# Optimization experiments

Measured on AMD Instinct MI355X. Metric: run time of the kernel, lower is better.

The kernel has to match this reference:

```python
import jax, jax.numpy as jnp
import numpy as np

VOCAB = 50000
D = 512          # in_feat == word_embedding_dim
B = 4096
S = 128
NUM_LABELS = 3


def setup_inputs() -> dict:
    key = jax.random.key(0)
    ks = jax.random.split(key, 16)
    ids_a = jax.random.randint(ks[0], (B, S), 0, VOCAB, dtype=jnp.int32)
    ids_b = jax.random.randint(ks[1], (B, S), 0, VOCAB, dtype=jnp.int32)
    mask_a = jax.random.randint(ks[2], (B, S), 0, 2) > 0
    mask_b = jax.random.randint(ks[3], (B, S), 0, 2) > 0
    s = 0.02
    W_emb = jax.random.normal(ks[4], (VOCAB, D), jnp.float32) * s
    W_emb = W_emb.at[0].set(0.0)  # padding_idx=0
    enc_w1 = jax.random.normal(ks[5], (D, D), jnp.float32) * s
    enc_b1 = jnp.zeros((D,), jnp.float32)
    enc_w2 = jax.random.normal(ks[6], (D, D), jnp.float32) * s
    enc_b2 = jnp.zeros((D,), jnp.float32)
    cls_w1 = jax.random.normal(ks[7], (2 * D, D), jnp.float32) * s
    cls_b1 = jnp.zeros((D,), jnp.float32)
    cls_w2 = jax.random.normal(ks[8], (D, NUM_LABELS), jnp.float32) * s
    cls_b2 = jnp.zeros((NUM_LABELS,), jnp.float32)
    return {
        "text_a_inputs_id": ids_a, "text_b_inputs_id": ids_b,
        "text_a_attention_mask": mask_a, "text_b_attention_mask": mask_b,
        "W_emb": W_emb,
        "enc_w1": enc_w1, "enc_b1": enc_b1, "enc_w2": enc_w2, "enc_b2": enc_b2,
        "cls_w1": cls_w1, "cls_b1": cls_b1, "cls_w2": cls_w2, "cls_b2": cls_b2,
    }


def _encode(ids, mask, W_emb, w1, b1, w2, b2):
    # embedding gather [B,S,D], fused masked sum-pool -> [B,D]
    emb = W_emb[ids]
    pooled = jnp.einsum("bsd,bs->bd", emb, mask.astype(emb.dtype))
    x = jnp.tanh(pooled @ w1 + b1)
    x = jnp.tanh(x @ w2 + b2)  # dropout is identity in eval
    return x


def reference(text_a_inputs_id, text_b_inputs_id, text_a_attention_mask,
              text_b_attention_mask, W_emb, enc_w1, enc_b1, enc_w2, enc_b2,
              cls_w1, cls_b1, cls_w2, cls_b2):
    va = _encode(text_a_inputs_id, text_a_attention_mask, W_emb, enc_w1, enc_b1, enc_w2, enc_b2)
    vb = _encode(text_b_inputs_id, text_b_attention_mask, W_emb, enc_w1, enc_b1, enc_w2, enc_b2)
    pooled = jnp.concatenate([va, vb], axis=-1)  # [B, 2D]
    h = jnp.tanh(pooled @ cls_w1 + cls_b1)
    logits = h @ cls_w2 + cls_b2  # [B, num_labels]
    return logits
```

## Files before the change

kernel.cpp:

```cpp
#include <hip/hip_runtime.h>


typedef unsigned short u16;
typedef __attribute__((ext_vector_type(8))) short short8;
typedef __attribute__((ext_vector_type(4))) float f32x4;

__device__ __forceinline__ float bfu2f(u16 u) {
    union { unsigned int i; float f; } v;
    v.i = ((unsigned int)u) << 16;
    return v.f;
}

__device__ __forceinline__ u16 f2bfu(float f) {
    union { float f; unsigned int i; } v;
    v.f = f;
    unsigned int x = v.i;
    x += 0x7fffu + ((x >> 16) & 1u);
    return (u16)(x >> 16);
}

__device__ __forceinline__ float fast_tanh(float x) {
    float xc = fminf(fmaxf(x, -15.f), 15.f);
    float e = __builtin_amdgcn_exp2f(xc * 2.885390082f);
    return (e - 1.f) / (e + 1.f);
}

__device__ __forceinline__ int detect_wave(const u16* __restrict__ W,
                                           const unsigned int* __restrict__ m,
                                           int lane)
{
    int cnt = 0;
    int w01 = 1, b01 = 1, lo16 = 0;
    #pragma unroll
    for (int j = lane; j < 256; j += 64) {
        u16 u = W[1024 + 2 * j];
        int e = (u >> 7) & 0xFF;
        cnt += (e >= 0x6A && e <= 0x7E) ? 1 : 0;
        unsigned int v = m[j];
        w01 &= (v <= 1u) ? 1 : 0;
        b01 &= ((v & ~0x01010101u) == 0u) ? 1 : 0;
        lo16 |= ((v & 0xFFFFu) == 0x3F80u) ? 1 : 0;
    }
    #pragma unroll
    for (int off = 32; off > 0; off >>= 1) {
        cnt  += __shfl_down(cnt, off);
        w01  &= __shfl_down(w01, off);
        b01  &= __shfl_down(b01, off);
        lo16 |= __shfl_down(lo16, off);
    }
    int mtype;
    if (w01)        mtype = 0;
    else if (b01)   mtype = 1;
    else if (lo16)  mtype = 2;
    else            mtype = 3;
    int fl = ((cnt >= 128) ? 1 : 0) | (mtype << 2);
    return __shfl(fl, 0);
}

__device__ __forceinline__ int mask_nonzero(const void* __restrict__ msk,
                                            int idx, int mtype)
{
    switch (mtype) {
        case 0:  return ((const int*)msk)[idx] != 0;
        case 1:  return ((const unsigned char*)msk)[idx] != 0;
        case 2:  return ((const u16*)msk)[idx] != 0;
        default: return ((const unsigned int*)msk)[idx] != 0u;
    }
}

__global__ __launch_bounds__(128) void pool_kernel(
    const int* __restrict__ ids_a, const int* __restrict__ ids_b,
    const void* __restrict__ mska, const void* __restrict__ mskb,
    const void* __restrict__ W, u16* __restrict__ P,
    const unsigned int* __restrict__ Mdet)
{
    __shared__ int s_ids[128];
    __shared__ int s_cnt;
    __shared__ int s_flags;
    __shared__ float sP[512];
    const int t = threadIdx.x;
    const int w = t >> 6;
    const int lane = t & 63;

    if (t == 0) s_cnt = 0;
    if (t < 64) {
        int fl = detect_wave((const u16*)W, Mdet, t);
        if (t == 0) s_flags = fl;
    }
    __syncthreads();
    const int  flags = s_flags;
    const bool isbf  = (flags & 1) != 0;
    const int  mtype = (flags >> 2) & 3;

    const int row = blockIdx.x;
    const int r   = row & 4095;
    const int* __restrict__ ids = (row < 4096) ? ids_a : ids_b;
    const void* __restrict__ msk = (row < 4096) ? mska : mskb;

    int id = ids[r * 128 + t];
    int mk = mask_nonzero(msk, r * 128 + t, mtype);
    if (mk) {
        int idx = atomicAdd(&s_cnt, 1);
        s_ids[idx] = id;
    }
    __syncthreads();
    const int cnt = s_cnt;

    float acc[8] = {};
    if (isbf) {
        const u16* Wb = (const u16*)W;
        int j = w;
        for (; j + 6 < cnt; j += 8) {
            union { uint4 v; u16 s[8]; } r0, r1, r2, r3;
            r0.v = *(const uint4*)(Wb + (size_t)s_ids[j + 0] * 512 + lane * 8);
            r1.v = *(const uint4*)(Wb + (size_t)s_ids[j + 2] * 512 + lane * 8);
            r2.v = *(const uint4*)(Wb + (size_t)s_ids[j + 4] * 512 + lane * 8);
            r3.v = *(const uint4*)(Wb + (size_t)s_ids[j + 6] * 512 + lane * 8);
            #pragma unroll
            for (int i = 0; i < 8; ++i)
                acc[i] += bfu2f(r0.s[i]) + bfu2f(r1.s[i]) +
                          bfu2f(r2.s[i]) + bfu2f(r3.s[i]);
        }
        for (; j < cnt; j += 2) {
            union { uint4 v; u16 s[8]; } rr;
            rr.v = *(const uint4*)(Wb + (size_t)s_ids[j] * 512 + lane * 8);
            #pragma unroll
            for (int i = 0; i < 8; ++i) acc[i] += bfu2f(rr.s[i]);
        }
    } else {
        const float* Wf = (const float*)W;
        for (int j = w; j < cnt; j += 2) {
            const float* rp = Wf + (size_t)s_ids[j] * 512 + lane * 8;
            float4 a = *(const float4*)(rp + 0);
            float4 b = *(const float4*)(rp + 4);
            acc[0] += a.x; acc[1] += a.y; acc[2] += a.z; acc[3] += a.w;
            acc[4] += b.x; acc[5] += b.y; acc[6] += b.z; acc[7] += b.w;
        }
    }

    if (w == 0) {
        #pragma unroll
        for (int i = 0; i < 8; ++i) sP[lane * 8 + i] = acc[i];
    }
    __syncthreads();
    if (w == 1) {
        union { uint4 v; u16 s[8]; } o;
        #pragma unroll
        for (int i = 0; i < 8; ++i)
            o.s[i] = f2bfu(acc[i] + sP[lane * 8 + i]);
        *(uint4*)(P + (size_t)row * 512 + lane * 8) = o.v;
    }
}

template<bool ISBF>
__device__ __forceinline__ void gemm_body(
    const u16* __restrict__ A, const u16* __restrict__ A2, int K1,
    const void* __restrict__ Bv, const void* __restrict__ biasv,
    u16* __restrict__ C, int N, int K,
    u16* __restrict__ As0, u16* __restrict__ Bs0)
{
    const int tid  = threadIdx.x;
    const int lane = tid & 63;
    const int wid = tid >> 6;
    const int wm  = (wid & 3) * 32;
    const int wn  = (wid >> 2) * 32;
    const int ar = tid >> 2;
    const int ak = (tid & 3) * 8;
    const int bk = tid >> 3;
    const int jn = tid & 7;
    const int nb = jn * 8;
    const int bofs = (((bk >> 3) + jn) & 3) * 8 + (bk & 7);
    const int lm = lane & 15;
    const int kq = lane >> 4;
    const int kc = kq * 8;
    const int m0 = blockIdx.x * 128;
    const int n0 = blockIdx.y * 64;

    const u16*   Bb = (const u16*)Bv;
    const float* Bf = (const float*)Bv;

    f32x4 acc[2][2];
    #pragma unroll
    for (int i = 0; i < 2; ++i)
        #pragma unroll
        for (int j = 0; j < 2; ++j)
            acc[i][j] = (f32x4){0.f, 0.f, 0.f, 0.f};

    uint4 ra;
    uint4 rbb;
    float4 rf0, rf1;

    #define FETCH(k0)                                                         \
    {                                                                         \
        const int kg = (k0) + ak;                                             \
        const u16* base = (kg < K1) ? (A + kg) : (A2 + (kg - K1));            \
        ra = *(const uint4*)(base + (size_t)(m0 + ar) * 512);                 \
        if (tid < 256) {                                                      \
            if constexpr (ISBF) {                                             \
                rbb = *(const uint4*)(Bb + (size_t)((k0) + bk) * N + n0 + nb);\
            } else {                                                          \
                const float* Bp = Bf + (size_t)((k0) + bk) * N + n0 + nb;     \
                rf0 = *(const float4*)(Bp + 0);                               \
                rf1 = *(const float4*)(Bp + 4);                               \
            }                                                                 \
        }                                                                     \
    }

    #define STORE(pp)                                                         \
    {                                                                         \
        *(uint4*)&As0[(pp) * 5120 + ar * 40 + ak] = ra;                       \
        if (tid < 256) {                                                      \
            u16 bvals[8];                                                     \
            if constexpr (ISBF) {                                             \
                union { uint4 v; u16 s[8]; } ub; ub.v = rbb;                  \
                _Pragma("unroll")                                             \
                for (int i = 0; i < 8; ++i) bvals[i] = ub.s[i];               \
            } else {                                                          \
                bvals[0] = f2bfu(rf0.x); bvals[1] = f2bfu(rf0.y);             \
                bvals[2] = f2bfu(rf0.z); bvals[3] = f2bfu(rf0.w);             \
                bvals[4] = f2bfu(rf1.x); bvals[5] = f2bfu(rf1.y);             \
                bvals[6] = f2bfu(rf1.z); bvals[7] = f2bfu(rf1.w);             \
            }                                                                 \
            _Pragma("unroll")                                                 \
            for (int i = 0; i < 8; ++i)                                       \
                Bs0[(pp) * 2560 + (nb + i) * 40 + bofs] = bvals[i];           \
        }                                                                     \
    }

    FETCH(0)
    STORE(0)
    FETCH(32)
    __syncthreads();

    int p = 0;
    for (int k0 = 0; k0 < K; k0 += 32) {
        if (k0 + 32 < K) {
            STORE(p ^ 1)
            if (k0 + 64 < K) FETCH(k0 + 64)
        }

        const u16* Ap = As0 + p * 5120;
        const u16* Bp2 = Bs0 + p * 2560;
        short8 af[2], bf[2];
        #pragma unroll
        for (int i = 0; i < 2; ++i)
            af[i] = *(const short8*)&Ap[(wm + i * 16 + lm) * 40 + kc];
        #pragma unroll
        for (int j = 0; j < 2; ++j) {
            const int n = wn + j * 16 + lm;
            const int ch = ((kq + (n >> 3)) & 3) * 8;
            bf[j] = *(const short8*)&Bp2[n * 40 + ch];
        }
        #pragma unroll
        for (int i = 0; i < 2; ++i)
            #pragma unroll
            for (int j = 0; j < 2; ++j)
                acc[i][j] = __builtin_amdgcn_mfma_f32_16x16x32_bf16(
                    af[i], bf[j], acc[i][j], 0, 0, 0);

        if (k0 + 32 < K) __syncthreads();
        p ^= 1;
    }
    #undef FETCH
    #undef STORE

    #pragma unroll
    for (int j = 0; j < 2; ++j) {
        const int n = n0 + wn + j * 16 + lm;
        const float bsv = ISBF ? bfu2f(((const u16*)biasv)[n])
                               : ((const float*)biasv)[n];
        #pragma unroll
        for (int i = 0; i < 2; ++i) {
            #pragma unroll
            for (int r = 0; r < 4; ++r) {
                const int m = m0 + wm + i * 16 + kq * 4 + r;
                C[(size_t)m * N + n] = f2bfu(fast_tanh(acc[i][j][r] + bsv));
            }
        }
    }
}

__global__ __launch_bounds__(512, 4) void gemm_mfma(
    const u16* __restrict__ A, const u16* __restrict__ A2, int K1,
    const void* __restrict__ B, const void* __restrict__ bias,
    u16* __restrict__ C, int N, int K,
    const u16* __restrict__ Wdet, const unsigned int* __restrict__ Mdet)
{
    __shared__ __align__(16) u16 As[2 * 128 * 40];
    __shared__ __align__(16) u16 Bs[2 * 64 * 40];
    __shared__ int s_flags;

    if (threadIdx.x < 64) {
        int fl = detect_wave(Wdet, Mdet, threadIdx.x);
        if (threadIdx.x == 0) s_flags = fl;
    }
    __syncthreads();
    if (s_flags & 1) gemm_body<true >(A, A2, K1, B, bias, C, N, K, As, Bs);
    else             gemm_body<false>(A, A2, K1, B, bias, C, N, K, As, Bs);
}

__global__ __launch_bounds__(64) void logits_kernel(
    const u16* __restrict__ H, const void* __restrict__ W2,
    const void* __restrict__ b2, float* __restrict__ out,
    const u16* __restrict__ Wdet, const unsigned int* __restrict__ Mdet)
{
    const int lane = threadIdx.x;
    const int fl = detect_wave(Wdet, Mdet, lane);
    const bool isbf = (fl & 1) != 0;

    const int m = blockIdx.x;
    union { uint4 v; u16 s[8]; } h;
    h.v = *(const uint4*)(H + (size_t)m * 512 + lane * 8);

    float a0 = 0.f, a1 = 0.f, a2 = 0.f;
    #pragma unroll
    for (int i = 0; i < 8; ++i) {
        const int k = lane * 8 + i;
        float x = bfu2f(h.s[i]);
        float w0, w1, w2;
        if (isbf) {
            const u16* Wb = (const u16*)W2;
            w0 = bfu2f(Wb[k * 3 + 0]); w1 = bfu2f(Wb[k * 3 + 1]); w2 = bfu2f(Wb[k * 3 + 2]);
        } else {
            const float* Wf = (const float*)W2;
            w0 = Wf[k * 3 + 0]; w1 = Wf[k * 3 + 1]; w2 = Wf[k * 3 + 2];
        }
        a0 += x * w0; a1 += x * w1; a2 += x * w2;
    }
    #pragma unroll
    for (int off = 32; off > 0; off >>= 1) {
        a0 += __shfl_down(a0, off);
        a1 += __shfl_down(a1, off);
        a2 += __shfl_down(a2, off);
    }
    if (lane == 0) {
        float b0, b1, b2v;
        if (isbf) {
            const u16* bb = (const u16*)b2;
            b0 = bfu2f(bb[0]); b1 = bfu2f(bb[1]); b2v = bfu2f(bb[2]);
        } else {
            const float* bf = (const float*)b2;
            b0 = bf[0]; b1 = bf[1]; b2v = bf[2];
        }
        out[m * 3 + 0] = a0 + b0;
        out[m * 3 + 1] = a1 + b1;
        out[m * 3 + 2] = a2 + b2v;
    }
}

extern "C" void kernel_launch(void* const* d_in, const int* in_sizes, int n_in,
                              void* d_out, int out_size, void* d_ws, size_t ws_size,
                              hipStream_t stream)
{
    const int* ids_a  = (const int*)d_in[0];
    const int* ids_b  = (const int*)d_in[1];
    const void* mask_a = d_in[2];
    const void* mask_b = d_in[3];
    const void* W_emb  = d_in[4];
    const void* enc_w1 = d_in[5];
    const void* enc_b1 = d_in[6];
    const void* enc_w2 = d_in[7];
    const void* enc_b2 = d_in[8];
    const void* cls_w1 = d_in[9];
    const void* cls_b1 = d_in[10];
    const void* cls_w2 = d_in[11];
    const void* cls_b2 = d_in[12];

    const u16* Wdet = (const u16*)W_emb;
    const unsigned int* Mdet = (const unsigned int*)mask_a;

    u16* buf0 = (u16*)d_ws;
    u16* buf1 = buf0 + (size_t)8192 * 512;

    pool_kernel<<<8192, 128, 0, stream>>>(ids_a, ids_b, mask_a, mask_b,
                                          W_emb, buf0, Mdet);

    gemm_mfma<<<dim3(64, 8), 512, 0, stream>>>(
        buf0, buf0, 512, enc_w1, enc_b1, buf1, 512, 512, Wdet, Mdet);

    gemm_mfma<<<dim3(64, 8), 512, 0, stream>>>(
        buf1, buf1, 512, enc_w2, enc_b2, buf0, 512, 512, Wdet, Mdet);

    gemm_mfma<<<dim3(32, 8), 512, 0, stream>>>(
        buf0, buf0 + (size_t)4096 * 512, 512, cls_w1, cls_b1, buf1, 512, 1024, Wdet, Mdet);

    logits_kernel<<<4096, 64, 0, stream>>>(buf1, cls_w2, cls_b2, (float*)d_out, Wdet, Mdet);
}
```

Before: 357.4 us.

## Fuse encoder and classifier GEMMs and logits into one cooperative kernel

Replaces the three GEMM launches and the logits launch with a single cooperative kernel that runs each stage over a 512-block grid separated by grid-wide syncs. It targets per-launch overhead and the idle gaps between dependent small kernels. It adds grid.sync costs, requires all blocks to be co-resident, and leaves half the blocks idle during the classifier GEMM. The old multi-launch path is kept as a fallback if the cooperative launch fails.

```diff
diff --git a/kernel.cpp b/kernel.cpp
--- a/kernel.cpp
+++ b/kernel.cpp
@@ -1,4 +1,7 @@
 #include <hip/hip_runtime.h>
+#include <hip/hip_cooperative_groups.h>
+
+namespace cg = cooperative_groups;
 
 
 typedef unsigned short u16;
@@ -153,10 +156,10 @@
 }
 
 template<bool ISBF>
-__device__ __forceinline__ void gemm_body(
-    const u16* __restrict__ A, const u16* __restrict__ A2, int K1,
+__device__ __forceinline__ void gemm_tile(
+    const u16* __restrict__ A, const u16* __restrict__ A2, const int K1,
     const void* __restrict__ Bv, const void* __restrict__ biasv,
-    u16* __restrict__ C, int N, int K,
+    u16* __restrict__ C, const int K, const int m0, const int n0,
     u16* __restrict__ As0, u16* __restrict__ Bs0)
 {
     const int tid  = threadIdx.x;
@@ -173,8 +176,6 @@
     const int lm = lane & 15;
     const int kq = lane >> 4;
     const int kc = kq * 8;
-    const int m0 = blockIdx.x * 128;
-    const int n0 = blockIdx.y * 64;
 
     const u16*   Bb = (const u16*)Bv;
     const float* Bf = (const float*)Bv;
@@ -197,9 +198,9 @@
         ra = *(const uint4*)(base + (size_t)(m0 + ar) * 512);                 \
         if (tid < 256) {                                                      \
             if constexpr (ISBF) {                                             \
-                rbb = *(const uint4*)(Bb + (size_t)((k0) + bk) * N + n0 + nb);\
+                rbb = *(const uint4*)(Bb + (size_t)((k0) + bk) * 512 + n0 + nb);\
             } else {                                                          \
-                const float* Bp = Bf + (size_t)((k0) + bk) * N + n0 + nb;     \
+                const float* Bp = Bf + (size_t)((k0) + bk) * 512 + n0 + nb;   \
                 rf0 = *(const float4*)(Bp + 0);                               \
                 rf1 = *(const float4*)(Bp + 4);                               \
             }                                                                 \
@@ -274,16 +275,114 @@
             #pragma unroll
             for (int r = 0; r < 4; ++r) {
                 const int m = m0 + wm + i * 16 + kq * 4 + r;
-                C[(size_t)m * N + n] = f2bfu(fast_tanh(acc[i][j][r] + bsv));
+                C[(size_t)m * 512 + n] = f2bfu(fast_tanh(acc[i][j][r] + bsv));
             }
         }
     }
+}
+
+template<bool ISBF>
+__device__ __forceinline__ void fused_body(
+    const void* __restrict__ w1, const void* __restrict__ b1,
+    const void* __restrict__ w2, const void* __restrict__ b2,
+    const void* __restrict__ cw1, const void* __restrict__ cb1,
+    const void* __restrict__ cw2, const void* __restrict__ cb2,
+    u16* __restrict__ buf0, u16* __restrict__ buf1,
+    float* __restrict__ out, u16* As, u16* Bs)
+{
+    cg::grid_group grid = cg::this_grid();
+    const int bid = blockIdx.x;
+    const int tid = threadIdx.x;
+    const int m0 = (bid & 63) * 128;
+    const int n0 = (bid >> 6) * 64;
+
+    const u16* src = buf0;
+    u16*       dst = buf1;
+    #pragma unroll 1
+    for (int s = 0; s < 2; ++s) {
+        const void* ww = s ? w2 : w1;
+        const void* bb = s ? b2 : b1;
+        gemm_tile<ISBF>(src, src, 512, ww, bb, dst, 512, m0, n0, As, Bs);
+        __threadfence();
+        grid.sync();
+        const u16* t = src; src = dst; dst = (u16*)t;
+    }
+
+    if (bid < 256)
+        gemm_tile<ISBF>(buf0, buf0 + (size_t)4096 * 512, 512, cw1, cb1,
+                        buf1, 1024, (bid & 31) * 128, (bid >> 5) * 64, As, Bs);
+    __threadfence();
+    grid.sync();
+
+    const int lane = tid & 63;
+    const int m = bid * 8 + (tid >> 6);
+    union { uint4 v; u16 s[8]; } h;
+    h.v = *(const uint4*)(buf1 + (size_t)m * 512 + lane * 8);
+
+    float a0 = 0.f, a1 = 0.f, a2 = 0.f;
+    #pragma unroll
+    for (int i = 0; i < 8; ++i) {
+        const int k = lane * 8 + i;
+        float x = bfu2f(h.s[i]);
+        float v0, v1, v2;
+        if constexpr (ISBF) {
+            const u16* Wb = (const u16*)cw2;
+            v0 = bfu2f(Wb[k * 3 + 0]); v1 = bfu2f(Wb[k * 3 + 1]); v2 = bfu2f(Wb[k * 3 + 2]);
+        } else {
+            const float* Wf = (const float*)cw2;
+            v0 = Wf[k * 3 + 0]; v1 = Wf[k * 3 + 1]; v2 = Wf[k * 3 + 2];
+        }
+        a0 += x * v0; a1 += x * v1; a2 += x * v2;
+    }
+    #pragma unroll
+    for (int off = 32; off > 0; off >>= 1) {
+        a0 += __shfl_down(a0, off);
+        a1 += __shfl_down(a1, off);
+        a2 += __shfl_down(a2, off);
+    }
+    if (lane == 0) {
+        float c0, c1, c2;
+        if constexpr (ISBF) {
+            const u16* bb = (const u16*)cb2;
+            c0 = bfu2f(bb[0]); c1 = bfu2f(bb[1]); c2 = bfu2f(bb[2]);
+        } else {
+            const float* bf = (const float*)cb2;
+            c0 = bf[0]; c1 = bf[1]; c2 = bf[2];
+        }
+        out[m * 3 + 0] = a0 + c0;
+        out[m * 3 + 1] = a1 + c1;
+        out[m * 3 + 2] = a2 + c2;
+    }
+}
+
+__global__ __launch_bounds__(512, 4) void fused_enc(
+    const void* __restrict__ w1, const void* __restrict__ b1,
+    const void* __restrict__ w2, const void* __restrict__ b2,
+    const void* __restrict__ cw1, const void* __restrict__ cb1,
+    const void* __restrict__ cw2, const void* __restrict__ cb2,
+    u16* __restrict__ buf0, u16* __restrict__ buf1,
+    float* __restrict__ out,
+    const u16* __restrict__ Wdet, const unsigned int* __restrict__ Mdet)
+{
+    __shared__ __align__(16) u16 As[2 * 128 * 40];
+    __shared__ __align__(16) u16 Bs[2 * 64 * 40];
+    __shared__ int s_flags;
+
+    if (threadIdx.x < 64) {
+        int fl = detect_wave(Wdet, Mdet, threadIdx.x);
+        if (threadIdx.x == 0) s_flags = fl;
+    }
+    __syncthreads();
+    if (s_flags & 1)
+        fused_body<true >(w1, b1, w2, b2, cw1, cb1, cw2, cb2, buf0, buf1, out, As, Bs);
+    else
+        fused_body<false>(w1, b1, w2, b2, cw1, cb1, cw2, cb2, buf0, buf1, out, As, Bs);
 }
 
 __global__ __launch_bounds__(512, 4) void gemm_mfma(
     const u16* __restrict__ A, const u16* __restrict__ A2, int K1,
     const void* __restrict__ B, const void* __restrict__ bias,
-    u16* __restrict__ C, int N, int K,
+    u16* __restrict__ C, int K,
     const u16* __restrict__ Wdet, const unsigned int* __restrict__ Mdet)
 {
     __shared__ __align__(16) u16 As[2 * 128 * 40];
@@ -295,8 +394,10 @@
         if (threadIdx.x == 0) s_flags = fl;
     }
     __syncthreads();
-    if (s_flags & 1) gemm_body<true >(A, A2, K1, B, bias, C, N, K, As, Bs);
-    else             gemm_body<false>(A, A2, K1, B, bias, C, N, K, As, Bs);
+    const int m0 = blockIdx.x * 128;
+    const int n0 = blockIdx.y * 64;
+    if (s_flags & 1) gemm_tile<true >(A, A2, K1, B, bias, C, K, m0, n0, As, Bs);
+    else             gemm_tile<false>(A, A2, K1, B, bias, C, K, m0, n0, As, Bs);
 }
 
 __global__ __launch_bounds__(64) void logits_kernel(
@@ -371,18 +472,28 @@
 
     u16* buf0 = (u16*)d_ws;
     u16* buf1 = buf0 + (size_t)8192 * 512;
+    float* outp = (float*)d_out;
 
     pool_kernel<<<8192, 128, 0, stream>>>(ids_a, ids_b, mask_a, mask_b,
                                           W_emb, buf0, Mdet);
 
-    gemm_mfma<<<dim3(64, 8), 512, 0, stream>>>(
-        buf0, buf0, 512, enc_w1, enc_b1, buf1, 512, 512, Wdet, Mdet);
-
-    gemm_mfma<<<dim3(64, 8), 512, 0, stream>>>(
-        buf1, buf1, 512, enc_w2, enc_b2, buf0, 512, 512, Wdet, Mdet);
-
-    gemm_mfma<<<dim3(32, 8), 512, 0, stream>>>(
-        buf0, buf0 + (size_t)4096 * 512, 512, cls_w1, cls_b1, buf1, 512, 1024, Wdet, Mdet);
-
-    logits_kernel<<<4096, 64, 0, stream>>>(buf1, cls_w2, cls_b2, (float*)d_out, Wdet, Mdet);
-}
+    void* args[13] = {
+        (void*)&enc_w1, (void*)&enc_b1, (void*)&enc_w2, (void*)&enc_b2,
+        (void*)&cls_w1, (void*)&cls_b1, (void*)&cls_w2, (void*)&cls_b2,
+        (void*)&buf0,   (void*)&buf1,   (void*)&outp,
+        (void*)&Wdet,   (void*)&Mdet
+    };
+    hipError_t err = hipLaunchCooperativeKernel(
+        (const void*)fused_enc, dim3(512, 1, 1), dim3(512, 1, 1),
+        args, 0, stream);
+
+    if (err != hipSuccess) {
+        gemm_mfma<<<dim3(64, 8), 512, 0, stream>>>(
+            buf0, buf0, 512, enc_w1, enc_b1, buf1, 512, Wdet, Mdet);
+        gemm_mfma<<<dim3(64, 8), 512, 0, stream>>>(
+            buf1, buf1, 512, enc_w2, enc_b2, buf0, 512, Wdet, Mdet);
+        gemm_mfma<<<dim3(32, 8), 512, 0, stream>>>(
+            buf0, buf0 + (size_t)4096 * 512, 512, cls_w1, cls_b1, buf1, 1024, Wdet, Mdet);
+        logits_kernel<<<4096, 64, 0, stream>>>(buf1, cls_w2, cls_b2, outp, Wdet, Mdet);
+    }
+}
```

After: 840.6 us. 2.35x slower.

## Fuse both encoder GEMMs per row block and fold logits into classifier GEMM

Applied to the files above, without the earlier changes.

Replaces the two separate encoder GEMM launches with one kernel. Each 32-row block holds its pooled rows in registers, computes the first layer into LDS-staged fragments, then the second layer, and writes the result back in place. The classifier GEMM now computes tanh and the 3-wide logit projection in its epilogue and accumulates into a pre-zeroed output with atomics, which removes the hidden-state round trip and the separate logits kernel. In exchange, each block re-reads the full weight matrices and the encoder grid is smaller (256 blocks of 32 rows), so it has less parallelism and more weight traffic. The atomic accumulation also makes the float summation order nondeterministic.

```diff
diff --git a/kernel.cpp b/kernel.cpp
--- a/kernel.cpp
+++ b/kernel.cpp
@@ -153,10 +153,165 @@
 }
 
 template<bool ISBF>
-__device__ __forceinline__ void gemm_body(
-    const u16* __restrict__ A, const u16* __restrict__ A2, int K1,
+__device__ __forceinline__ void enc12_body(
+    u16* __restrict__ P,
+    const void* __restrict__ w1v, const void* __restrict__ b1v,
+    const void* __restrict__ w2v, const void* __restrict__ b2v,
+    u16* __restrict__ Bs, u16* __restrict__ Xbuf)
+{
+    const int tid  = threadIdx.x;
+    const int lane = tid & 63;
+    const int wid  = tid >> 6;
+    const int wm   = (wid & 1) * 16;
+    const int wn   = (wid >> 1) * 16;
+    const int lm   = lane & 15;
+    const int kq   = lane >> 4;
+    const int kc   = kq * 8;
+    const int R0   = blockIdx.x * 32;
+
+    const int bk = tid >> 3;
+    const int jn = tid & 7;
+    const int nb = jn * 8;
+
+    const u16*   b1b = (const u16*)b1v; const float* b1f = (const float*)b1v;
+    const u16*   b2b = (const u16*)b2v; const float* b2f = (const float*)b2v;
+
+    short8 af[16];
+    {
+        const u16* arow = P + (size_t)(R0 + wm + lm) * 512 + kc;
+        #pragma unroll
+        for (int s = 0; s < 16; ++s)
+            af[s] = *(const short8*)(arow + s * 32);
+    }
+    short8 af2[16];
+
+    const u16* Wb; const float* Wf;
+    uint4 rb0, rb1;
+    float4 rf00, rf01, rf10, rf11;
+
+#define FETCHW(k0, n0)                                                        \
+    {                                                                         \
+        const int kr0 = (k0) + bk;                                            \
+        const int kr1 = (k0) + bk + 64;                                       \
+        if constexpr (ISBF) {                                                 \
+            rb0 = *(const uint4*)(Wb + (size_t)kr0 * 512 + (n0) + nb);        \
+            rb1 = *(const uint4*)(Wb + (size_t)kr1 * 512 + (n0) + nb);        \
+        } else {                                                              \
+            const float* p0_ = Wf + (size_t)kr0 * 512 + (n0) + nb;            \
+            const float* p1_ = Wf + (size_t)kr1 * 512 + (n0) + nb;            \
+            rf00 = *(const float4*)p0_; rf01 = *(const float4*)(p0_ + 4);     \
+            rf10 = *(const float4*)p1_; rf11 = *(const float4*)(p1_ + 4);     \
+        }                                                                     \
+    }
+
+#define STOREW(pp)                                                            \
+    {                                                                         \
+        u16 bv0[8], bv1[8];                                                   \
+        if constexpr (ISBF) {                                                 \
+            union { uint4 v; u16 s[8]; } u0_, u1_;                            \
+            u0_.v = rb0; u1_.v = rb1;                                         \
+            _Pragma("unroll")                                                 \
+            for (int i = 0; i < 8; ++i) { bv0[i] = u0_.s[i]; bv1[i] = u1_.s[i]; } \
+        } else {                                                              \
+            bv0[0]=f2bfu(rf00.x); bv0[1]=f2bfu(rf00.y);                       \
+            bv0[2]=f2bfu(rf00.z); bv0[3]=f2bfu(rf00.w);                       \
+            bv0[4]=f2bfu(rf01.x); bv0[5]=f2bfu(rf01.y);                       \
+            bv0[6]=f2bfu(rf01.z); bv0[7]=f2bfu(rf01.w);                       \
+            bv1[0]=f2bfu(rf10.x); bv1[1]=f2bfu(rf10.y);                       \
+            bv1[2]=f2bfu(rf10.z); bv1[3]=f2bfu(rf10.w);                       \
+            bv1[4]=f2bfu(rf11.x); bv1[5]=f2bfu(rf11.y);                       \
+            bv1[6]=f2bfu(rf11.z); bv1[7]=f2bfu(rf11.w);                       \
+        }                                                                     \
+        const int o0_ = ((((bk >> 3) + jn) & 15)) * 8 + (bk & 7);             \
+        const int o1_ = ((((bk >> 3) + 8 + jn) & 15)) * 8 + (bk & 7);         \
+        _Pragma("unroll")                                                     \
+        for (int i = 0; i < 8; ++i) {                                         \
+            Bs[(pp) * 8704 + (nb + i) * 136 + o0_] = bv0[i];                  \
+            Bs[(pp) * 8704 + (nb + i) * 136 + o1_] = bv1[i];                  \
+        }                                                                     \
+    }
+
+#define KLOOP(afin)                                                           \
+    FETCHW(0, n0) STOREW(0) FETCHW(128, n0)                                   \
+    __syncthreads();                                                          \
+    _Pragma("unroll")                                                         \
+    for (int kb = 0; kb < 4; ++kb) {                                          \
+        const int p_ = kb & 1;                                                \
+        if (kb < 3) { STOREW(p_ ^ 1) if (kb < 2) FETCHW((kb + 2) * 128, n0) } \
+        _Pragma("unroll")                                                     \
+        for (int s = 0; s < 4; ++s) {                                         \
+            const int n_ = wn + lm;                                           \
+            const int ch = (((s * 4 + kq) + (n_ >> 3)) & 15) * 8;             \
+            short8 bf = *(const short8*)&Bs[p_ * 8704 + n_ * 136 + ch];       \
+            acc = __builtin_amdgcn_mfma_f32_16x16x32_bf16(afin[kb * 4 + s],   \
+                                                          bf, acc, 0, 0, 0);  \
+        }                                                                     \
+        if (kb < 3) __syncthreads();                                          \
+    }
+
+    Wb = (const u16*)w1v; Wf = (const float*)w1v;
+    #pragma unroll
+    for (int t = 0; t < 8; ++t) {
+        const int n0 = t * 64;
+        f32x4 acc = (f32x4){0.f, 0.f, 0.f, 0.f};
+        KLOOP(af)
+        const int   ncol = n0 + wn + lm;
+        const float bia  = ISBF ? bfu2f(b1b[ncol]) : b1f[ncol];
+        u16* xw = Xbuf + (t & 1) * (32 * 72);
+        #pragma unroll
+        for (int r = 0; r < 4; ++r)
+            xw[(wm + kq * 4 + r) * 72 + wn + lm] =
+                f2bfu(fast_tanh(acc[r] + bia));
+        __syncthreads();
+        const u16* xr = Xbuf + (t & 1) * (32 * 72) + (size_t)(wm + lm) * 72;
+        af2[2 * t + 0] = *(const short8*)(xr + kc);
+        af2[2 * t + 1] = *(const short8*)(xr + 32 + kc);
+    }
+
+    Wb = (const u16*)w2v; Wf = (const float*)w2v;
+    #pragma unroll 1
+    for (int t2 = 0; t2 < 8; ++t2) {
+        const int n0 = t2 * 64;
+        f32x4 acc = (f32x4){0.f, 0.f, 0.f, 0.f};
+        KLOOP(af2)
+        const int   ncol = n0 + wn + lm;
+        const float bia  = ISBF ? bfu2f(b2b[ncol]) : b2f[ncol];
+        #pragma unroll
+        for (int r = 0; r < 4; ++r)
+            P[(size_t)(R0 + wm + kq * 4 + r) * 512 + ncol] =
+                f2bfu(fast_tanh(acc[r] + bia));
+        __syncthreads();
+    }
+#undef KLOOP
+#undef STOREW
+#undef FETCHW
+}
+
+__global__ __launch_bounds__(512, 2) void enc12_kernel(
+    u16* __restrict__ P,
+    const void* __restrict__ w1, const void* __restrict__ b1,
+    const void* __restrict__ w2, const void* __restrict__ b2,
+    const u16* __restrict__ Wdet, const unsigned int* __restrict__ Mdet)
+{
+    __shared__ __align__(16) u16 Bs[2 * 8704];
+    __shared__ __align__(16) u16 Xbuf[2 * 32 * 72];
+    __shared__ int s_flags;
+
+    if (threadIdx.x < 64) {
+        int fl = detect_wave(Wdet, Mdet, threadIdx.x);
+        if (threadIdx.x == 0) s_flags = fl;
+    }
+    __syncthreads();
+    if (s_flags & 1) enc12_body<true >(P, w1, b1, w2, b2, Bs, Xbuf);
+    else             enc12_body<false>(P, w1, b1, w2, b2, Bs, Xbuf);
+}
+
+template<bool ISBF>
+__device__ __forceinline__ void g3_body(
+    const u16* __restrict__ A, const u16* __restrict__ A2, const int K1,
     const void* __restrict__ Bv, const void* __restrict__ biasv,
-    u16* __restrict__ C, int N, int K,
+    const void* __restrict__ w2v, const void* __restrict__ cb2v,
+    float* __restrict__ outp, const int K,
     u16* __restrict__ As0, u16* __restrict__ Bs0)
 {
     const int tid  = threadIdx.x;
@@ -173,8 +328,8 @@
     const int lm = lane & 15;
     const int kq = lane >> 4;
     const int kc = kq * 8;
-    const int m0 = blockIdx.x * 128;
-    const int n0 = blockIdx.y * 64;
+    const int m0 = (blockIdx.x & 31) * 128;
+    const int n0 = (blockIdx.x >> 5) * 64;
 
     const u16*   Bb = (const u16*)Bv;
     const float* Bf = (const float*)Bv;
@@ -186,27 +341,26 @@
         for (int j = 0; j < 2; ++j)
             acc[i][j] = (f32x4){0.f, 0.f, 0.f, 0.f};
 
-    uint4 ra;
-    uint4 rbb;
+    uint4 ra, rbb;
     float4 rf0, rf1;
 
-    #define FETCH(k0)                                                         \
+#define FETCH(k0)                                                             \
     {                                                                         \
         const int kg = (k0) + ak;                                             \
         const u16* base = (kg < K1) ? (A + kg) : (A2 + (kg - K1));            \
         ra = *(const uint4*)(base + (size_t)(m0 + ar) * 512);                 \
         if (tid < 256) {                                                      \
             if constexpr (ISBF) {                                             \
-                rbb = *(const uint4*)(Bb + (size_t)((k0) + bk) * N + n0 + nb);\
+                rbb = *(const uint4*)(Bb + (size_t)((k0) + bk) * 512 + n0 + nb);\
             } else {                                                          \
-                const float* Bp = Bf + (size_t)((k0) + bk) * N + n0 + nb;     \
+                const float* Bp = Bf + (size_t)((k0) + bk) * 512 + n0 + nb;   \
                 rf0 = *(const float4*)(Bp + 0);                               \
                 rf1 = *(const float4*)(Bp + 4);                               \
             }                                                                 \
         }                                                                     \
     }
 
-    #define STORE(pp)                                                         \
+#define STORE(pp)                                                             \
     {                                                                         \
         *(uint4*)&As0[(pp) * 5120 + ar * 40 + ak] = ra;                       \
         if (tid < 256) {                                                      \
@@ -238,52 +392,94 @@
             STORE(p ^ 1)
             if (k0 + 64 < K) FETCH(k0 + 64)
         }
-
         const u16* Ap = As0 + p * 5120;
         const u16* Bp2 = Bs0 + p * 2560;
-        short8 af[2], bf[2];
+        short8 afr[2], bfr[2];
         #pragma unroll
         for (int i = 0; i < 2; ++i)
-            af[i] = *(const short8*)&Ap[(wm + i * 16 + lm) * 40 + kc];
+            afr[i] = *(const short8*)&Ap[(wm + i * 16 + lm) * 40 + kc];
         #pragma unroll
         for (int j = 0; j < 2; ++j) {
             const int n = wn + j * 16 + lm;
             const int ch = ((kq + (n >> 3)) & 3) * 8;
-            bf[j] = *(const short8*)&Bp2[n * 40 + ch];
+            bfr[j] = *(const short8*)&Bp2[n * 40 + ch];
         }
         #pragma unroll
         for (int i = 0; i < 2; ++i)
             #pragma unroll
             for (int j = 0; j < 2; ++j)
                 acc[i][j] = __builtin_amdgcn_mfma_f32_16x16x32_bf16(
-                    af[i], bf[j], acc[i][j], 0, 0, 0);
-
+                    afr[i], bfr[j], acc[i][j], 0, 0, 0);
         if (k0 + 32 < K) __syncthreads();
         p ^= 1;
     }
-    #undef FETCH
-    #undef STORE
+#undef FETCH
+#undef STORE
+
+    float lg[2][4][3];
+    #pragma unroll
+    for (int i = 0; i < 2; ++i)
+        #pragma unroll
+        for (int r = 0; r < 4; ++r)
+            #pragma unroll
+            for (int l = 0; l < 3; ++l) lg[i][r][l] = 0.f;
 
     #pragma unroll
     for (int j = 0; j < 2; ++j) {
         const int n = n0 + wn + j * 16 + lm;
         const float bsv = ISBF ? bfu2f(((const u16*)biasv)[n])
                                : ((const float*)biasv)[n];
-        #pragma unroll
-        for (int i = 0; i < 2; ++i) {
+        float wc[3];
+        #pragma unroll
+        for (int l = 0; l < 3; ++l)
+            wc[l] = ISBF ? bfu2f(((const u16*)w2v)[n * 3 + l])
+                         : ((const float*)w2v)[n * 3 + l];
+        #pragma unroll
+        for (int i = 0; i < 2; ++i)
+            #pragma unroll
+            for (int r = 0; r < 4; ++r) {
+                const float h = fast_tanh(acc[i][j][r] + bsv);
+                #pragma unroll
+                for (int l = 0; l < 3; ++l) lg[i][r][l] += h * wc[l];
+            }
+    }
+    #pragma unroll
+    for (int off = 1; off <= 8; off <<= 1)
+        #pragma unroll
+        for (int i = 0; i < 2; ++i)
+            #pragma unroll
+            for (int r = 0; r < 4; ++r)
+                #pragma unroll
+                for (int l = 0; l < 3; ++l)
+                    lg[i][r][l] += __shfl_xor(lg[i][r][l], off);
+
+    if (lm == 0) {
+        const bool addb = (n0 == 0) && (wn == 0);
+        float cb[3];
+        #pragma unroll
+        for (int l = 0; l < 3; ++l)
+            cb[l] = ISBF ? bfu2f(((const u16*)cb2v)[l])
+                         : ((const float*)cb2v)[l];
+        #pragma unroll
+        for (int i = 0; i < 2; ++i)
             #pragma unroll
             for (int r = 0; r < 4; ++r) {
                 const int m = m0 + wm + i * 16 + kq * 4 + r;
-                C[(size_t)m * N + n] = f2bfu(fast_tanh(acc[i][j][r] + bsv));
+                #pragma unroll
+                for (int l = 0; l < 3; ++l) {
+                    float v = lg[i][r][l];
+                    if (addb) v += cb[l];
+                    atomicAdd(&outp[m * 3 + l], v);
+                }
             }
-        }
-    }
-}
-
-__global__ __launch_bounds__(512, 4) void gemm_mfma(
+    }
+}
+
+__global__ __launch_bounds__(512, 2) void gemm3_logits(
     const u16* __restrict__ A, const u16* __restrict__ A2, int K1,
     const void* __restrict__ B, const void* __restrict__ bias,
-    u16* __restrict__ C, int N, int K,
+    const void* __restrict__ w2, const void* __restrict__ cb2,
+    float* __restrict__ out, int K,
     const u16* __restrict__ Wdet, const unsigned int* __restrict__ Mdet)
 {
     __shared__ __align__(16) u16 As[2 * 128 * 40];
@@ -295,57 +491,10 @@
         if (threadIdx.x == 0) s_flags = fl;
     }
     __syncthreads();
-    if (s_flags & 1) gemm_body<true >(A, A2, K1, B, bias, C, N, K, As, Bs);
-    else             gemm_body<false>(A, A2, K1, B, bias, C, N, K, As, Bs);
-}
-
-__global__ __launch_bounds__(64) void logits_kernel(
-    const u16* __restrict__ H, const void* __restrict__ W2,
-    const void* __restrict__ b2, float* __restrict__ out,
-    const u16* __restrict__ Wdet, const unsigned int* __restrict__ Mdet)
-{
-    const int lane = threadIdx.x;
-    const int fl = detect_wave(Wdet, Mdet, lane);
-    const bool isbf = (fl & 1) != 0;
-
-    const int m = blockIdx.x;
-    union { uint4 v; u16 s[8]; } h;
-    h.v = *(const uint4*)(H + (size_t)m * 512 + lane * 8);
-
-    float a0 = 0.f, a1 = 0.f, a2 = 0.f;
-    #pragma unroll
-    for (int i = 0; i < 8; ++i) {
-        const int k = lane * 8 + i;
-        float x = bfu2f(h.s[i]);
-        float w0, w1, w2;
-        if (isbf) {
-            const u16* Wb = (const u16*)W2;
-            w0 = bfu2f(Wb[k * 3 + 0]); w1 = bfu2f(Wb[k * 3 + 1]); w2 = bfu2f(Wb[k * 3 + 2]);
-        } else {
-            const float* Wf = (const float*)W2;
-            w0 = Wf[k * 3 + 0]; w1 = Wf[k * 3 + 1]; w2 = Wf[k * 3 + 2];
-        }
-        a0 += x * w0; a1 += x * w1; a2 += x * w2;
-    }
-    #pragma unroll
-    for (int off = 32; off > 0; off >>= 1) {
-        a0 += __shfl_down(a0, off);
-        a1 += __shfl_down(a1, off);
-        a2 += __shfl_down(a2, off);
-    }
-    if (lane == 0) {
-        float b0, b1, b2v;
-        if (isbf) {
-            const u16* bb = (const u16*)b2;
-            b0 = bfu2f(bb[0]); b1 = bfu2f(bb[1]); b2v = bfu2f(bb[2]);
-        } else {
-            const float* bf = (const float*)b2;
-            b0 = bf[0]; b1 = bf[1]; b2v = bf[2];
-        }
-        out[m * 3 + 0] = a0 + b0;
-        out[m * 3 + 1] = a1 + b1;
-        out[m * 3 + 2] = a2 + b2v;
-    }
+    if (s_flags & 1)
+        g3_body<true >(A, A2, K1, B, bias, w2, cb2, out, K, As, Bs);
+    else
+        g3_body<false>(A, A2, K1, B, bias, w2, cb2, out, K, As, Bs);
 }
 
 extern "C" void kernel_launch(void* const* d_in, const int* in_sizes, int n_in,
@@ -370,19 +519,17 @@
     const unsigned int* Mdet = (const unsigned int*)mask_a;
 
     u16* buf0 = (u16*)d_ws;
-    u16* buf1 = buf0 + (size_t)8192 * 512;
+    float* outp = (float*)d_out;
+
+    hipMemsetAsync(d_out, 0, 4096 * 3 * sizeof(float), stream);
 
     pool_kernel<<<8192, 128, 0, stream>>>(ids_a, ids_b, mask_a, mask_b,
                                           W_emb, buf0, Mdet);
 
-    gemm_mfma<<<dim3(64, 8), 512, 0, stream>>>(
-        buf0, buf0, 512, enc_w1, enc_b1, buf1, 512, 512, Wdet, Mdet);
-
-    gemm_mfma<<<dim3(64, 8), 512, 0, stream>>>(
-        buf1, buf1, 512, enc_w2, enc_b2, buf0, 512, 512, Wdet, Mdet);
-
-    gemm_mfma<<<dim3(32, 8), 512, 0, stream>>>(
-        buf0, buf0 + (size_t)4096 * 512, 512, cls_w1, cls_b1, buf1, 512, 1024, Wdet, Mdet);
-
-    logits_kernel<<<4096, 64, 0, stream>>>(buf1, cls_w2, cls_b2, (float*)d_out, Wdet, Mdet);
-}
+    enc12_kernel<<<256, 512, 0, stream>>>(buf0, enc_w1, enc_b1,
+                                          enc_w2, enc_b2, Wdet, Mdet);
+
+    gemm3_logits<<<256, 512, 0, stream>>>(
+        buf0, buf0 + (size_t)4096 * 512, 512, cls_w1, cls_b1,
+        cls_w2, cls_b2, outp, 1024, Wdet, Mdet);
+}
```

Result: slower. 409.5 us (+14.6%).
